# Kernel optimization log

Hardware: AMD Instinct MI355X
Metric: run time of the kernel (lower is better)

The kernel has to match this reference:

```python
import jax, jax.numpy as jnp
import numpy as np

B, C, H, V = 16384, 5, 256, 512
NUM_ITER = 2


def setup_inputs() -> dict:
    key = jax.random.key(0)
    k1, k2, k3, k4 = jax.random.split(key, 4)
    # v0: one-hot categorical visible units, shape [B, C, V, 1]
    idx = jax.random.randint(k1, (B, V), 0, C)
    v0 = jax.nn.one_hot(idx, C, axis=1, dtype=jnp.float32)[..., None]
    W = 0.01 * jax.random.normal(k2, (C, H, V), dtype=jnp.float32)
    b = 0.01 * jax.random.normal(k3, (C, V, 1), dtype=jnp.float32)
    c = 0.01 * jax.random.normal(k4, (H, 1), dtype=jnp.float32)
    return {"v0": v0, "W": W, "b": b, "c": c, "num_sampling_iter": NUM_ITER}


def reference(v0, W, b, c, num_sampling_iter):
    key = jax.random.key(42)
    b2 = b[..., 0]   # [C, V]
    c1 = c[:, 0]     # [H]
    v = v0[..., 0]   # [B, C, V]

    def sample_h(k, v):
        # p(h=1|v) = sigmoid(sum_c W[c] @ v[:,c] + c)
        p = jax.nn.sigmoid(jnp.einsum('chv,bcv->bh', W, v) + c1)  # [B, H]
        return jax.random.bernoulli(k, p).astype(v.dtype)

    def sample_v(k, h):
        # logits over categories per visible unit: W[c].T @ h + b[c]
        logits = jnp.einsum('chv,bh->bcv', W, h) + b2  # [B, C, V]
        idx = jax.random.categorical(k, logits, axis=1)  # [B, V]
        return jax.nn.one_hot(idx, C, axis=1, dtype=h.dtype)  # [B, C, V]

    keys = jax.random.split(key, 2 * num_sampling_iter + 1)
    h = sample_h(keys[0], v)
    h_given_v0 = h
    for i in range(num_sampling_iter):  # small fixed iteration count
        v = sample_v(keys[2 * i + 1], h)
        h = sample_h(keys[2 * i + 2], v)
    return (v[..., None], h[..., None], h_given_v0[..., None])
```

## Files before the change

kernel.cpp:

```cpp
#include <hip/hip_runtime.h>
#include <cstdint>
#include <cstddef>


#define B_DIM 16384
#define C_DIM 5
#define H_DIM 256
#define V_DIM 512
#define KC    320

struct TFOut { uint32_t a, b; };

typedef float f32x2 __attribute__((ext_vector_type(2)));

#if __has_builtin(__builtin_elementwise_fma)
#define PKFMA(A, B, C) __builtin_elementwise_fma((A), (B), (C))
#else
static __device__ inline f32x2 pkfma_(f32x2 a, f32x2 b, f32x2 c) {
  f32x2 r; r.x = fmaf(a.x, b.x, c.x); r.y = fmaf(a.y, b.y, c.y); return r;
}
#define PKFMA(A, B, C) pkfma_((A), (B), (C))
#endif

__host__ __device__ static inline TFOut tf2x32(uint32_t k0, uint32_t k1,
                                               uint32_t c0, uint32_t c1) {
  uint32_t ks2 = k0 ^ k1 ^ 0x1BD11BDAu;
  uint32_t x0 = c0 + k0, x1 = c1 + k1;
#define TF_R(r) { x0 += x1; x1 = (x1 << r) | (x1 >> (32 - r)); x1 ^= x0; }
  TF_R(13) TF_R(15) TF_R(26) TF_R(6)
  x0 += k1;  x1 += ks2 + 1u;
  TF_R(17) TF_R(29) TF_R(16) TF_R(24)
  x0 += ks2; x1 += k0 + 2u;
  TF_R(13) TF_R(15) TF_R(26) TF_R(6)
  x0 += k0;  x1 += k1 + 3u;
  TF_R(17) TF_R(29) TF_R(16) TF_R(24)
  x0 += k1;  x1 += ks2 + 4u;
  TF_R(13) TF_R(15) TF_R(26) TF_R(6)
  x0 += ks2; x1 += k0 + 5u;
#undef TF_R
  TFOut o; o.a = x0; o.b = x1; return o;
}

__device__ static inline uint32_t rng_bits(uint32_t k0, uint32_t k1, uint32_t i) {
  TFOut r = tf2x32(k0, k1, 0u, i);
  return r.a ^ r.b;
}

__device__ static inline float bits_to_unit_float(uint32_t bits) {
  return __uint_as_float((bits >> 9) | 0x3F800000u) - 1.0f;
}

__device__ static float xla_exp(float x_in) {
#pragma clang fp contract(off)
  float x = fminf(x_in, 88.3762626647950f);
  x = fmaxf(x, -88.3762626647949f);
  float fx = floorf(x * 1.44269504088896341f + 0.5f);
  float tmp = fx * 0.693359375f;
  float z = fx * -2.12194440e-4f;
  x = x - tmp;
  x = x - z;
  z = x * x;
  float y = 1.9875691500e-4f;
  y = y * x + 1.3981999507e-3f;
  y = y * x + 8.3334519073e-3f;
  y = y * x + 4.1665795894e-2f;
  y = y * x + 1.6666665459e-1f;
  y = y * x + 5.0000001201e-1f;
  y = y * z + x;
  y = y + 1.0f;
  int n = (int)fx;
  y = y * __uint_as_float((uint32_t)(n + 127) << 23);
  return y;
}

__device__ static float xla_log(float x_in) {
#pragma clang fp contract(off)
  float xv = fmaxf(x_in, 1.17549435e-38f);
  uint32_t bits = __float_as_uint(xv);
  float e = (float)((int)(bits >> 23) - 126);
  float x = __uint_as_float((bits & 0x007FFFFFu) | 0x3F000000u);
  bool m = (x < 0.707106781186547524f);
  float tmp = m ? x : 0.0f;
  x = x - 1.0f;
  e = e - (m ? 1.0f : 0.0f);
  x = x + tmp;
  float z = x * x;
  float y = 7.0376836292e-2f;
  y = y * x + -1.1514610310e-1f;
  y = y * x + 1.1676998740e-1f;
  y = y * x + -1.2420140846e-1f;
  y = y * x + 1.4249322787e-1f;
  y = y * x + -1.6668057665e-1f;
  y = y * x + 2.0000714765e-1f;
  y = y * x + -2.4999993993e-1f;
  y = y * x + 3.3333331174e-1f;
  y = y * x;
  y = y * z;
  float t1 = e * -2.12194440e-4f;
  y = y + t1;
  float t2 = z * 0.5f;
  y = y - t2;
  x = x + y;
  float t3 = e * 0.693359375f;
  x = x + t3;
  return x;
}


__global__ void k_sentinel(float* out, float d) {
  out[0] = d;
}

__global__ __launch_bounds__(256) void k_idx(const float* __restrict__ v0,
                                             uint8_t* __restrict__ idx) {
  int t = blockIdx.x * 256 + threadIdx.x;
  int b = t >> 9, v = t & 511;
  const float* p = v0 + (size_t)b * (C_DIM * V_DIM) + v;
  int cf = 0;
#pragma unroll
  for (int c = 0; c < C_DIM; ++c)
    if (p[c * V_DIM] > 0.5f) cf = c;
  idx[t] = (uint8_t)cf;
}

__global__ __launch_bounds__(256) void k_wt(const float* __restrict__ W,
                                            float* __restrict__ Wt) {
  int t = blockIdx.x * 256 + threadIdx.x;
  int h = t & 255; int rest = t >> 8; int v = rest & 511; int c = rest >> 9;
  Wt[t] = W[((size_t)c * H_DIM + h) * V_DIM + v];
}

__global__ __launch_bounds__(256) void k_sample_h(
    const float* __restrict__ Wt, const float* __restrict__ c1,
    const uint8_t* __restrict__ idx,
    float* __restrict__ out_h, uint32_t* __restrict__ out_mask,
    uint32_t key0, uint32_t key1) {
  __shared__ uint8_t  sidx[V_DIM];
  __shared__ uint32_t soff[V_DIM];
  __shared__ uint16_t cnt[8][5];
  __shared__ uint16_t base[8][5];
  __shared__ uint16_t jb[10];
  int b = blockIdx.x;
  int t = threadIdx.x;
  if (t < 128)
    ((uint32_t*)sidx)[t] = ((const uint32_t*)(idx + (size_t)b * V_DIM))[t];
  __syncthreads();

  int lane = t & 63, wv = t >> 6;
  int v0 = t,       c0 = sidx[v0];
  int v1 = t + 256, c1i = sidx[v1];
  int rank0, rank1;
  {
    unsigned long long bal[5];
#pragma unroll
    for (int cc = 0; cc < 5; ++cc) bal[cc] = __ballot(c0 == cc);
    if (lane == 0) {
#pragma unroll
      for (int cc = 0; cc < 5; ++cc) cnt[wv][cc] = (uint16_t)__popcll(bal[cc]);
    }
    rank0 = (int)__popcll(bal[c0] & ((1ull << lane) - 1ull));
  }
  {
    unsigned long long bal[5];
#pragma unroll
    for (int cc = 0; cc < 5; ++cc) bal[cc] = __ballot(c1i == cc);
    if (lane == 0) {
#pragma unroll
      for (int cc = 0; cc < 5; ++cc) cnt[4 + wv][cc] = (uint16_t)__popcll(bal[cc]);
    }
    rank1 = (int)__popcll(bal[c1i] & ((1ull << lane) - 1ull));
  }
  __syncthreads();
  if (t == 0) {
    int pos = 0;
    for (int cc = 0; cc < 5; ++cc)
      for (int g = 0; g < 8; ++g) { base[g][cc] = (uint16_t)pos; pos += cnt[g][cc]; }
  }
  __syncthreads();
  soff[base[wv][c0] + rank0]       = (uint32_t)(c0 * V_DIM + v0) << 10;
  soff[base[4 + wv][c1i] + rank1]  = (uint32_t)(c1i * V_DIM + v1) << 10;
  __syncthreads();
  if (t < 10) {
    uint32_t target = (uint32_t)(t * KC) << 10;
    int lo = 0, hi = V_DIM;
    while (lo < hi) { int mid = (lo + hi) >> 1;
      if (soff[mid] < target) lo = mid + 1; else hi = mid; }
    jb[t] = (uint16_t)lo;
  }
  __syncthreads();

  const char* Wh = (const char*)Wt + (size_t)t * 4;
  float total = 0.0f;
  for (int s = 0; s < 9; ++s) {
    int j = jb[s], jend = jb[s + 1];
    float psum = 0.0f;
    for (; j + 4 <= jend; j += 4) {
      float w0 = *(const float*)(Wh + soff[j]);
      float w1 = *(const float*)(Wh + soff[j + 1]);
      float w2 = *(const float*)(Wh + soff[j + 2]);
      float w3 = *(const float*)(Wh + soff[j + 3]);
      psum += w0; psum += w1; psum += w2; psum += w3;
    }
    for (; j < jend; ++j) psum += *(const float*)(Wh + soff[j]);
    total += psum;
  }

  float tt = total + c1[t];
  float p = 1.0f / (1.0f + xla_exp(-tt));

  uint32_t i = (uint32_t)(b * H_DIM + t);
  float u = bits_to_unit_float(rng_bits(key0, key1, i));
  bool hb = (u < p);
  if (out_h) out_h[(size_t)b * H_DIM + t] = hb ? 1.0f : 0.0f;

  unsigned long long m = __ballot(hb);
  if ((t & 63) == 0) {
    out_mask[(size_t)b * 8 + wv * 2 + 0] = (uint32_t)(m & 0xFFFFFFFFull);
    out_mask[(size_t)b * 8 + wv * 2 + 1] = (uint32_t)(m >> 32);
  }
}

#define ACC_H(BITS, W4)                                              \
  {                                                                  \
    f32x2 w01 = {(W4).x, (W4).y}, w23 = {(W4).z, (W4).w};            \
    uint32_t bits_ = (BITS) >> (bgrp * 8);                           \
    _Pragma("unroll")                                                \
    for (int i = 0; i < 8; ++i) {                                    \
      float f = (float)((bits_ >> i) & 1u);                          \
      f32x2 ff = {f, f};                                             \
      a01[i] = PKFMA(w01, ff, a01[i]);                               \
      a23[i] = PKFMA(w23, ff, a23[i]);                               \
    }                                                                \
  }

__global__ __launch_bounds__(256, 4) void k_sample_v(
    const float* __restrict__ W, const float* __restrict__ b2,
    const uint32_t* __restrict__ mask, uint8_t* __restrict__ idx_out,
    uint32_t key0, uint32_t key1) {
  __shared__ uint32_t smask[16][8];
  __shared__ __align__(16) uint32_t tb[H_DIM];
  int tid = threadIdx.x;
  int b0 = blockIdx.x * 16;

  if (tid < 128) smask[tid >> 3][tid & 7] = mask[(size_t)b0 * 8 + tid];
  __syncthreads();
  {
    int h = tid;
    uint32_t w = (uint32_t)(h >> 5), s = (uint32_t)(h & 31), x = 0;
#pragma unroll
    for (int j = 0; j < 16; ++j)
      x |= ((smask[j][w] >> s) & 1u) << j;
    tb[h] = x;
  }
  __syncthreads();

  int wv = tid >> 6, lane = tid & 63;
  int bgrp = wv & 1, vhalf = wv >> 1;
  int b_base = b0 + bgrp * 8;
  int v0 = vhalf * 256 + lane * 4;

  float best[8][4];
  uint32_t bc[8];
#pragma unroll
  for (int i = 0; i < 8; ++i) bc[i] = 0u;

  const uint4* tbv = (const uint4*)tb;

  for (int c = 0; c < C_DIM; ++c) {
    f32x2 a01[8], a23[8];
#pragma unroll
    for (int i = 0; i < 8; ++i) {
      a01[i] = (f32x2){0.0f, 0.0f};
      a23[i] = (f32x2){0.0f, 0.0f};
    }
    const float* wp = W + (size_t)c * (H_DIM * V_DIM) + v0;
    uint4 qn = tbv[0];
    for (int h4 = 0; h4 < 64; ++h4) {
      uint4 qq = qn;
      if (h4 < 63) qn = tbv[h4 + 1];
      float4 w0 = *(const float4*)(wp);
      float4 w1 = *(const float4*)(wp + V_DIM);
      float4 w2 = *(const float4*)(wp + 2 * V_DIM);
      float4 w3 = *(const float4*)(wp + 3 * V_DIM);
      wp += 4 * V_DIM;
      ACC_H(qq.x, w0)
      ACC_H(qq.y, w1)
      ACC_H(qq.z, w2)
      ACC_H(qq.w, w3)
    }

    float4 bv = *(const float4*)(b2 + c * V_DIM + v0);
    float bb0 = bv.x, bb1 = bv.y, bb2 = bv.z, bb3 = bv.w;
#pragma unroll
    for (int i = 0; i < 8; ++i) {
      uint32_t ib = ((uint32_t)(b_base + i) * C_DIM + (uint32_t)c) * V_DIM
                    + (uint32_t)v0;
      float av[4] = {a01[i].x, a01[i].y, a23[i].x, a23[i].y};
      float bbq[4] = {bb0, bb1, bb2, bb3};
#pragma unroll
      for (int q = 0; q < 4; ++q) {
        float uf = bits_to_unit_float(rng_bits(key0, key1, ib + (uint32_t)q));
        if (uf == 0.0f) uf = 1.17549435e-38f;
        float g = -xla_log(-xla_log(uf));
        float z = g + (av[q] + bbq[q]);
        if (c == 0 || z > best[i][q]) {
          best[i][q] = z;
          bc[i] = (bc[i] & ~(0xFFu << (8 * q))) | ((uint32_t)c << (8 * q));
        }
      }
    }
  }

#pragma unroll
  for (int i = 0; i < 8; ++i)
    *(uint32_t*)(idx_out + (size_t)(b_base + i) * V_DIM + v0) = bc[i];
}

__global__ __launch_bounds__(256) void k_onehot(const uint8_t* __restrict__ idx,
                                                float* __restrict__ out) {
  int t = blockIdx.x * 256 + threadIdx.x;
  int v = t & 511; int rest = t >> 9; int c = rest % C_DIM; int b = rest / C_DIM;
  out[t] = (idx[(size_t)b * V_DIM + v] == c) ? 1.0f : 0.0f;
}


extern "C" void kernel_launch(void* const* d_in, const int* in_sizes, int n_in,
                              void* d_out, int out_size, void* d_ws, size_t ws_size,
                              hipStream_t stream) {
  float* out = (float*)d_out;

  const size_t WS_NEED = 2621440ull
                       + 2621440ull
                       + 8388608ull
                       + 524288ull;
  float D = 0.0f;
  if (n_in < 4)                       D = 910.0f + (float)n_in;
  else if (in_sizes[0] != 41943040)   D = 920.0f;
  else if (in_sizes[1] != 655360)     D = 921.0f;
  else if (in_sizes[2] != 2560)       D = 922.0f;
  else if (in_sizes[3] != 256)        D = 923.0f;
  else if (out_size != 50331648)      D = 930.0f + (float)out_size * 1e-6f;
  else if (ws_size < WS_NEED)         D = 100.0f + (float)(ws_size >> 20);
  if (D != 0.0f) {
    hipLaunchKernelGGL(k_sentinel, dim3(1), dim3(1), 0, stream, out, D);
    return;
  }

  const float* v0 = (const float*)d_in[0];
  const float* W  = (const float*)d_in[1];
  const float* b2 = (const float*)d_in[2];
  const float* c1 = (const float*)d_in[3];

  float* out_v  = out;
  float* out_h  = out + (size_t)B_DIM * C_DIM * V_DIM;
  float* out_h0 = out_h + (size_t)B_DIM * H_DIM;

  char* ws = (char*)d_ws;
  float*    Wt   = (float*)(ws);
  uint8_t*  idx  = (uint8_t*)(ws + 5242880);
  uint32_t* mask = (uint32_t*)(ws + 13631488);

  uint32_t keys[5][2];
  for (int i = 0; i < 5; ++i) {
    TFOut r = tf2x32(0u, 42u, 0u, (uint32_t)i);
    keys[i][0] = r.a; keys[i][1] = r.b;
  }

  hipLaunchKernelGGL(k_wt,  dim3(2560),  dim3(256), 0, stream, W, Wt);
  hipLaunchKernelGGL(k_idx, dim3(32768), dim3(256), 0, stream, v0, idx);

  hipLaunchKernelGGL(k_sample_h, dim3(B_DIM), dim3(256), 0, stream,
                     Wt, c1, idx, out_h0, mask, keys[0][0], keys[0][1]);
  hipLaunchKernelGGL(k_sample_v, dim3(B_DIM / 16), dim3(256), 0, stream,
                     W, b2, mask, idx, keys[1][0], keys[1][1]);
  hipLaunchKernelGGL(k_sample_h, dim3(B_DIM), dim3(256), 0, stream,
                     Wt, c1, idx, (float*)nullptr, mask, keys[2][0], keys[2][1]);
  hipLaunchKernelGGL(k_sample_v, dim3(B_DIM / 16), dim3(256), 0, stream,
                     W, b2, mask, idx, keys[3][0], keys[3][1]);
  hipLaunchKernelGGL(k_sample_h, dim3(B_DIM), dim3(256), 0, stream,
                     Wt, c1, idx, out_h, mask, keys[4][0], keys[4][1]);
  hipLaunchKernelGGL(k_onehot, dim3(163840), dim3(256), 0, stream, idx, out_v);
}
```

Before: 2.223 ms.

## Tile sample_h over 16-row batches with shared W slabs; split sample_v into GEMM and Gumbel

k_sample_h now handles 16 batch rows and half of H per block. It streams Wt through double-buffered shared-memory slabs so each weight chunk is reused across 16 rows instead of gathered per row from global memory. sample_v is split into a plain GEMM kernel that writes the logits into the output buffer, followed by a separate elementwise Gumbel-argmax kernel. This trades the fused compute for extra global traffic on an intermediate of about 168 MB. The new h kernel's per-row while loops over shared memory and its many syncs may introduce divergence and barrier overhead.

```diff
diff --git a/kernel.cpp b/kernel.cpp
--- a/kernel.cpp
+++ b/kernel.cpp
@@ -7,20 +7,8 @@
 #define C_DIM 5
 #define H_DIM 256
 #define V_DIM 512
-#define KC    320
 
 struct TFOut { uint32_t a, b; };
-
-typedef float f32x2 __attribute__((ext_vector_type(2)));
-
-#if __has_builtin(__builtin_elementwise_fma)
-#define PKFMA(A, B, C) __builtin_elementwise_fma((A), (B), (C))
-#else
-static __device__ inline f32x2 pkfma_(f32x2 a, f32x2 b, f32x2 c) {
-  f32x2 r; r.x = fmaf(a.x, b.x, c.x); r.y = fmaf(a.y, b.y, c.y); return r;
-}
-#define PKFMA(A, B, C) pkfma_((A), (B), (C))
-#endif
 
 __host__ __device__ static inline TFOut tf2x32(uint32_t k0, uint32_t k1,
                                                uint32_t c0, uint32_t c1) {
@@ -130,190 +118,238 @@
   Wt[t] = W[((size_t)c * H_DIM + h) * V_DIM + v];
 }
 
-__global__ __launch_bounds__(256) void k_sample_h(
-    const float* __restrict__ Wt, const float* __restrict__ c1,
+__global__ __launch_bounds__(256, 4) void k_sample_h(
+    const float* __restrict__ Wt, const float* __restrict__ c1g,
     const uint8_t* __restrict__ idx,
     float* __restrict__ out_h, uint32_t* __restrict__ out_mask,
     uint32_t key0, uint32_t key1) {
   __shared__ uint8_t  sidx[V_DIM];
-  __shared__ uint32_t soff[V_DIM];
+  __shared__ uint16_t soff[16][V_DIM];
+  __shared__ __align__(16) float slab[2][16 * 128];
   __shared__ uint16_t cnt[8][5];
   __shared__ uint16_t base[8][5];
-  __shared__ uint16_t jb[10];
-  int b = blockIdx.x;
+  __shared__ uint32_t hb32[16][4];
+
   int t = threadIdx.x;
-  if (t < 128)
-    ((uint32_t*)sidx)[t] = ((const uint32_t*)(idx + (size_t)b * V_DIM))[t];
+  int bb = blockIdx.x >> 1, hh = blockIdx.x & 1;
+  int b0 = bb * 16, h0 = hh * 128;
+  int wv = t >> 6, lane = t & 63;
+
+  for (int bi = 0; bi < 16; ++bi) {
+    if (t < 128)
+      ((uint32_t*)sidx)[t] =
+          ((const uint32_t*)(idx + (size_t)(b0 + bi) * V_DIM))[t];
+    __syncthreads();
+    int v0 = t, c0 = sidx[v0];
+    int v1 = t + 256, c1i = sidx[v1];
+    int rank0, rank1;
+    {
+      unsigned long long bal[5];
+#pragma unroll
+      for (int cc = 0; cc < 5; ++cc) bal[cc] = __ballot(c0 == cc);
+      if (lane == 0) {
+#pragma unroll
+        for (int cc = 0; cc < 5; ++cc) cnt[wv][cc] = (uint16_t)__popcll(bal[cc]);
+      }
+      rank0 = (int)__popcll(bal[c0] & ((1ull << lane) - 1ull));
+    }
+    {
+      unsigned long long bal[5];
+#pragma unroll
+      for (int cc = 0; cc < 5; ++cc) bal[cc] = __ballot(c1i == cc);
+      if (lane == 0) {
+#pragma unroll
+        for (int cc = 0; cc < 5; ++cc) cnt[4 + wv][cc] = (uint16_t)__popcll(bal[cc]);
+      }
+      rank1 = (int)__popcll(bal[c1i] & ((1ull << lane) - 1ull));
+    }
+    __syncthreads();
+    if (t == 0) {
+      int pos = 0;
+      for (int cc = 0; cc < 5; ++cc)
+        for (int gg = 0; gg < 8; ++gg) { base[gg][cc] = (uint16_t)pos; pos += cnt[gg][cc]; }
+    }
+    __syncthreads();
+    soff[bi][base[wv][c0] + rank0]      = (uint16_t)(c0 * V_DIM + v0);
+    soff[bi][base[4 + wv][c1i] + rank1] = (uint16_t)(c1i * V_DIM + v1);
+    __syncthreads();
+  }
+
+  float ps0[4], ps1[4], tt0[4], tt1[4];
+  int jp[4];
+#pragma unroll
+  for (int i = 0; i < 4; ++i) {
+    ps0[i] = 0.f; ps1[i] = 0.f; tt0[i] = 0.f; tt1[i] = 0.f; jp[i] = 0;
+  }
+
+  {
+    int p = t * 4;
+    int row = p >> 7, off = p & 127;
+    const float* s = Wt + (size_t)row * H_DIM + h0 + off;
+    float4 r0 = *(const float4*)s;
+    float4 r1 = *(const float4*)(s + 8 * H_DIM);
+    *(float4*)&slab[0][row * 128 + off] = r0;
+    *(float4*)&slab[0][(row + 8) * 128 + off] = r1;
+  }
   __syncthreads();
 
-  int lane = t & 63, wv = t >> 6;
-  int v0 = t,       c0 = sidx[v0];
-  int v1 = t + 256, c1i = sidx[v1];
-  int rank0, rank1;
-  {
-    unsigned long long bal[5];
-#pragma unroll
-    for (int cc = 0; cc < 5; ++cc) bal[cc] = __ballot(c0 == cc);
-    if (lane == 0) {
-#pragma unroll
-      for (int cc = 0; cc < 5; ++cc) cnt[wv][cc] = (uint16_t)__popcll(bal[cc]);
-    }
-    rank0 = (int)__popcll(bal[c0] & ((1ull << lane) - 1ull));
-  }
-  {
-    unsigned long long bal[5];
-#pragma unroll
-    for (int cc = 0; cc < 5; ++cc) bal[cc] = __ballot(c1i == cc);
-    if (lane == 0) {
-#pragma unroll
-      for (int cc = 0; cc < 5; ++cc) cnt[4 + wv][cc] = (uint16_t)__popcll(bal[cc]);
-    }
-    rank1 = (int)__popcll(bal[c1i] & ((1ull << lane) - 1ull));
-  }
+  for (int ch = 0; ch < 160; ++ch) {
+    int buf = ch & 1;
+    float4 r0, r1; int row = 0, off = 0;
+    bool pre = (ch + 1 < 160);
+    if (pre) {
+      int p = t * 4;
+      row = p >> 7; off = p & 127;
+      const float* s = Wt + ((size_t)(ch + 1) * 16 + row) * H_DIM + h0 + off;
+      r0 = *(const float4*)s;
+      r1 = *(const float4*)(s + 8 * H_DIM);
+    }
+    if ((ch % 20) == 0) {
+#pragma unroll
+      for (int i = 0; i < 4; ++i) {
+        tt0[i] = tt0[i] + ps0[i]; ps0[i] = 0.f;
+        tt1[i] = tt1[i] + ps1[i]; ps1[i] = 0.f;
+      }
+    }
+    int kend = ch * 16 + 16;
+#pragma unroll
+    for (int i = 0; i < 4; ++i) {
+      int bi = wv * 4 + i;
+      int j = jp[i];
+      float p0 = ps0[i], p1 = ps1[i];
+      while (j < 512) {
+        int k = soff[bi][j];
+        if (k >= kend) break;
+        const float* wp = &slab[buf][(k & 15) * 128 + (lane << 1)];
+        float2 w2 = *(const float2*)wp;
+        p0 += w2.x;
+        p1 += w2.y;
+        ++j;
+      }
+      ps0[i] = p0; ps1[i] = p1; jp[i] = j;
+    }
+    __syncthreads();
+    if (pre) {
+      *(float4*)&slab[buf ^ 1][row * 128 + off] = r0;
+      *(float4*)&slab[buf ^ 1][(row + 8) * 128 + off] = r1;
+    }
+    __syncthreads();
+  }
+#pragma unroll
+  for (int i = 0; i < 4; ++i) {
+    tt0[i] = tt0[i] + ps0[i];
+    tt1[i] = tt1[i] + ps1[i];
+  }
+
+  if (t < 64) ((uint32_t*)hb32)[t] = 0u;
   __syncthreads();
-  if (t == 0) {
-    int pos = 0;
-    for (int cc = 0; cc < 5; ++cc)
-      for (int g = 0; g < 8; ++g) { base[g][cc] = (uint16_t)pos; pos += cnt[g][cc]; }
+  float2 c1v = *(const float2*)&c1g[h0 + (lane << 1)];
+  int h = h0 + (lane << 1);
+#pragma unroll
+  for (int i = 0; i < 4; ++i) {
+    int b = b0 + wv * 4 + i;
+    float ta = tt0[i] + c1v.x;
+    float tb = tt1[i] + c1v.y;
+    float pa = 1.0f / (1.0f + xla_exp(-ta));
+    float pb = 1.0f / (1.0f + xla_exp(-tb));
+    float ua = bits_to_unit_float(rng_bits(key0, key1, (uint32_t)(b * H_DIM + h)));
+    float ub = bits_to_unit_float(rng_bits(key0, key1, (uint32_t)(b * H_DIM + h + 1)));
+    bool ha = ua < pa, hb = ub < pb;
+    if (out_h) {
+      float2 o; o.x = ha ? 1.0f : 0.0f; o.y = hb ? 1.0f : 0.0f;
+      *(float2*)&out_h[(size_t)b * H_DIM + h] = o;
+    }
+    uint32_t bitpos = (uint32_t)((lane << 1) & 31);
+    uint32_t val = ((ha ? 1u : 0u) << bitpos) | ((hb ? 1u : 0u) << (bitpos + 1));
+    atomicOr(&hb32[wv * 4 + i][lane >> 4], val);
   }
   __syncthreads();
-  soff[base[wv][c0] + rank0]       = (uint32_t)(c0 * V_DIM + v0) << 10;
-  soff[base[4 + wv][c1i] + rank1]  = (uint32_t)(c1i * V_DIM + v1) << 10;
-  __syncthreads();
-  if (t < 10) {
-    uint32_t target = (uint32_t)(t * KC) << 10;
-    int lo = 0, hi = V_DIM;
-    while (lo < hi) { int mid = (lo + hi) >> 1;
-      if (soff[mid] < target) lo = mid + 1; else hi = mid; }
-    jb[t] = (uint16_t)lo;
-  }
-  __syncthreads();
-
-  const char* Wh = (const char*)Wt + (size_t)t * 4;
-  float total = 0.0f;
-  for (int s = 0; s < 9; ++s) {
-    int j = jb[s], jend = jb[s + 1];
-    float psum = 0.0f;
-    for (; j + 4 <= jend; j += 4) {
-      float w0 = *(const float*)(Wh + soff[j]);
-      float w1 = *(const float*)(Wh + soff[j + 1]);
-      float w2 = *(const float*)(Wh + soff[j + 2]);
-      float w3 = *(const float*)(Wh + soff[j + 3]);
-      psum += w0; psum += w1; psum += w2; psum += w3;
-    }
-    for (; j < jend; ++j) psum += *(const float*)(Wh + soff[j]);
-    total += psum;
-  }
-
-  float tt = total + c1[t];
-  float p = 1.0f / (1.0f + xla_exp(-tt));
-
-  uint32_t i = (uint32_t)(b * H_DIM + t);
-  float u = bits_to_unit_float(rng_bits(key0, key1, i));
-  bool hb = (u < p);
-  if (out_h) out_h[(size_t)b * H_DIM + t] = hb ? 1.0f : 0.0f;
-
-  unsigned long long m = __ballot(hb);
-  if ((t & 63) == 0) {
-    out_mask[(size_t)b * 8 + wv * 2 + 0] = (uint32_t)(m & 0xFFFFFFFFull);
-    out_mask[(size_t)b * 8 + wv * 2 + 1] = (uint32_t)(m >> 32);
-  }
-}
-
-#define ACC_H(BITS, W4)                                              \
-  {                                                                  \
-    f32x2 w01 = {(W4).x, (W4).y}, w23 = {(W4).z, (W4).w};            \
-    uint32_t bits_ = (BITS) >> (bgrp * 8);                           \
-    _Pragma("unroll")                                                \
-    for (int i = 0; i < 8; ++i) {                                    \
-      float f = (float)((bits_ >> i) & 1u);                          \
-      f32x2 ff = {f, f};                                             \
-      a01[i] = PKFMA(w01, ff, a01[i]);                               \
-      a23[i] = PKFMA(w23, ff, a23[i]);                               \
-    }                                                                \
-  }
-
-__global__ __launch_bounds__(256, 4) void k_sample_v(
-    const float* __restrict__ W, const float* __restrict__ b2,
-    const uint32_t* __restrict__ mask, uint8_t* __restrict__ idx_out,
-    uint32_t key0, uint32_t key1) {
+  if (t < 64) {
+    int bl = t >> 2, wl = t & 3;
+    out_mask[(size_t)(b0 + bl) * 8 + hh * 4 + wl] = hb32[bl][wl];
+  }
+}
+
+#define GEMM_PAIR(i, F)                      \
+  a0[i] = fmaf(w2.x, F, a0[i]);              \
+  a1[i] = fmaf(w2.y, F, a1[i]);
+
+__global__ __launch_bounds__(256, 4) void k_gemm_v(
+    const float* __restrict__ W, const uint32_t* __restrict__ mask,
+    float* __restrict__ sums) {
   __shared__ uint32_t smask[16][8];
-  __shared__ __align__(16) uint32_t tb[H_DIM];
-  int tid = threadIdx.x;
+  __shared__ __align__(16) float tbf[H_DIM][16];
+  int t = threadIdx.x;
   int b0 = blockIdx.x * 16;
-
-  if (tid < 128) smask[tid >> 3][tid & 7] = mask[(size_t)b0 * 8 + tid];
+  if (t < 128) smask[t >> 3][t & 7] = mask[(size_t)b0 * 8 + t];
   __syncthreads();
   {
-    int h = tid;
+    int h = t;
     uint32_t w = (uint32_t)(h >> 5), s = (uint32_t)(h & 31), x = 0;
 #pragma unroll
     for (int j = 0; j < 16; ++j)
       x |= ((smask[j][w] >> s) & 1u) << j;
-    tb[h] = x;
+#pragma unroll
+    for (int i = 0; i < 16; ++i)
+      tbf[h][i] = (float)((x >> i) & 1u);
   }
   __syncthreads();
 
-  int wv = tid >> 6, lane = tid & 63;
-  int bgrp = wv & 1, vhalf = wv >> 1;
-  int b_base = b0 + bgrp * 8;
-  int v0 = vhalf * 256 + lane * 4;
-
-  float best[8][4];
-  uint32_t bc[8];
-#pragma unroll
-  for (int i = 0; i < 8; ++i) bc[i] = 0u;
-
-  const uint4* tbv = (const uint4*)tb;
+  int wv = t >> 6, lane = t & 63;
+  int v0 = wv * 128 + (lane << 1);
 
   for (int c = 0; c < C_DIM; ++c) {
-    f32x2 a01[8], a23[8];
-#pragma unroll
-    for (int i = 0; i < 8; ++i) {
-      a01[i] = (f32x2){0.0f, 0.0f};
-      a23[i] = (f32x2){0.0f, 0.0f};
-    }
+    float a0[16], a1[16];
+#pragma unroll
+    for (int i = 0; i < 16; ++i) { a0[i] = 0.f; a1[i] = 0.f; }
     const float* wp = W + (size_t)c * (H_DIM * V_DIM) + v0;
-    uint4 qn = tbv[0];
-    for (int h4 = 0; h4 < 64; ++h4) {
-      uint4 qq = qn;
-      if (h4 < 63) qn = tbv[h4 + 1];
-      float4 w0 = *(const float4*)(wp);
-      float4 w1 = *(const float4*)(wp + V_DIM);
-      float4 w2 = *(const float4*)(wp + 2 * V_DIM);
-      float4 w3 = *(const float4*)(wp + 3 * V_DIM);
-      wp += 4 * V_DIM;
-      ACC_H(qq.x, w0)
-      ACC_H(qq.y, w1)
-      ACC_H(qq.z, w2)
-      ACC_H(qq.w, w3)
-    }
-
-    float4 bv = *(const float4*)(b2 + c * V_DIM + v0);
-    float bb0 = bv.x, bb1 = bv.y, bb2 = bv.z, bb3 = bv.w;
-#pragma unroll
-    for (int i = 0; i < 8; ++i) {
-      uint32_t ib = ((uint32_t)(b_base + i) * C_DIM + (uint32_t)c) * V_DIM
-                    + (uint32_t)v0;
-      float av[4] = {a01[i].x, a01[i].y, a23[i].x, a23[i].y};
-      float bbq[4] = {bb0, bb1, bb2, bb3};
-#pragma unroll
-      for (int q = 0; q < 4; ++q) {
-        float uf = bits_to_unit_float(rng_bits(key0, key1, ib + (uint32_t)q));
-        if (uf == 0.0f) uf = 1.17549435e-38f;
-        float g = -xla_log(-xla_log(uf));
-        float z = g + (av[q] + bbq[q]);
-        if (c == 0 || z > best[i][q]) {
-          best[i][q] = z;
-          bc[i] = (bc[i] & ~(0xFFu << (8 * q))) | ((uint32_t)c << (8 * q));
-        }
+#pragma unroll 2
+    for (int h = 0; h < H_DIM; ++h) {
+      float2 w2 = *(const float2*)wp;
+      wp += V_DIM;
+      const float4* fp = (const float4*)&tbf[h][0];
+      float4 fA = fp[0], fB = fp[1], fC = fp[2], fD = fp[3];
+      GEMM_PAIR(0,  fA.x) GEMM_PAIR(1,  fA.y) GEMM_PAIR(2,  fA.z) GEMM_PAIR(3,  fA.w)
+      GEMM_PAIR(4,  fB.x) GEMM_PAIR(5,  fB.y) GEMM_PAIR(6,  fB.z) GEMM_PAIR(7,  fB.w)
+      GEMM_PAIR(8,  fC.x) GEMM_PAIR(9,  fC.y) GEMM_PAIR(10, fC.z) GEMM_PAIR(11, fC.w)
+      GEMM_PAIR(12, fD.x) GEMM_PAIR(13, fD.y) GEMM_PAIR(14, fD.z) GEMM_PAIR(15, fD.w)
+    }
+#pragma unroll
+    for (int i = 0; i < 16; ++i) {
+      float2 o; o.x = a0[i]; o.y = a1[i];
+      *(float2*)&sums[((size_t)c * B_DIM + b0 + i) * V_DIM + v0] = o;
+    }
+  }
+}
+
+__global__ __launch_bounds__(256, 4) void k_gumbel_v(
+    const float* __restrict__ sums, const float* __restrict__ b2,
+    uint8_t* __restrict__ idx_out, uint32_t key0, uint32_t key1) {
+  int gidx = blockIdx.x * 256 + threadIdx.x;
+  int b = gidx >> 7;
+  int v0 = (gidx & 127) << 2;
+  float best[4];
+  uint32_t bc = 0;
+#pragma unroll
+  for (int c = 0; c < C_DIM; ++c) {
+    float4 av = *(const float4*)&sums[((size_t)c * B_DIM + b) * V_DIM + v0];
+    float4 bv = *(const float4*)&b2[c * V_DIM + v0];
+    uint32_t ib = ((uint32_t)b * C_DIM + (uint32_t)c) * V_DIM + (uint32_t)v0;
+    float avq[4] = {av.x, av.y, av.z, av.w};
+    float bvq[4] = {bv.x, bv.y, bv.z, bv.w};
+#pragma unroll
+    for (int q = 0; q < 4; ++q) {
+      float uf = bits_to_unit_float(rng_bits(key0, key1, ib + (uint32_t)q));
+      if (uf == 0.0f) uf = 1.17549435e-38f;
+      float gz = -xla_log(-xla_log(uf));
+      float z = gz + (avq[q] + bvq[q]);
+      if (c == 0 || z > best[q]) {
+        best[q] = z;
+        bc = (bc & ~(0xFFu << (8 * q))) | ((uint32_t)c << (8 * q));
       }
     }
   }
-
-#pragma unroll
-  for (int i = 0; i < 8; ++i)
-    *(uint32_t*)(idx_out + (size_t)(b_base + i) * V_DIM + v0) = bc[i];
+  *(uint32_t*)(idx_out + (size_t)b * V_DIM + v0) = bc;
 }
 
 __global__ __launch_bounds__(256) void k_onehot(const uint8_t* __restrict__ idx,
@@ -360,6 +396,8 @@
   uint8_t*  idx  = (uint8_t*)(ws + 5242880);
   uint32_t* mask = (uint32_t*)(ws + 13631488);
 
+  float* sums = out_v;
+
   uint32_t keys[5][2];
   for (int i = 0; i < 5; ++i) {
     TFOut r = tf2x32(0u, 42u, 0u, (uint32_t)i);
@@ -369,15 +407,19 @@
   hipLaunchKernelGGL(k_wt,  dim3(2560),  dim3(256), 0, stream, W, Wt);
   hipLaunchKernelGGL(k_idx, dim3(32768), dim3(256), 0, stream, v0, idx);
 
-  hipLaunchKernelGGL(k_sample_h, dim3(B_DIM), dim3(256), 0, stream,
+  hipLaunchKernelGGL(k_sample_h, dim3(B_DIM / 16 * 2), dim3(256), 0, stream,
                      Wt, c1, idx, out_h0, mask, keys[0][0], keys[0][1]);
-  hipLaunchKernelGGL(k_sample_v, dim3(B_DIM / 16), dim3(256), 0, stream,
-                     W, b2, mask, idx, keys[1][0], keys[1][1]);
-  hipLaunchKernelGGL(k_sample_h, dim3(B_DIM), dim3(256), 0, stream,
+  hipLaunchKernelGGL(k_gemm_v, dim3(B_DIM / 16), dim3(256), 0, stream,
+                     W, mask, sums);
+  hipLaunchKernelGGL(k_gumbel_v, dim3(B_DIM * 128 / 256), dim3(256), 0, stream,
+                     sums, b2, idx, keys[1][0], keys[1][1]);
+  hipLaunchKernelGGL(k_sample_h, dim3(B_DIM / 16 * 2), dim3(256), 0, stream,
                      Wt, c1, idx, (float*)nullptr, mask, keys[2][0], keys[2][1]);
-  hipLaunchKernelGGL(k_sample_v, dim3(B_DIM / 16), dim3(256), 0, stream,
-                     W, b2, mask, idx, keys[3][0], keys[3][1]);
-  hipLaunchKernelGGL(k_sample_h, dim3(B_DIM), dim3(256), 0, stream,
+  hipLaunchKernelGGL(k_gemm_v, dim3(B_DIM / 16), dim3(256), 0, stream,
+                     W, mask, sums);
+  hipLaunchKernelGGL(k_gumbel_v, dim3(B_DIM * 128 / 256), dim3(256), 0, stream,
+                     sums, b2, idx, keys[3][0], keys[3][1]);
+  hipLaunchKernelGGL(k_sample_h, dim3(B_DIM / 16 * 2), dim3(256), 0, stream,
                      Wt, c1, idx, out_h, mask, keys[4][0], keys[4][1]);
   hipLaunchKernelGGL(k_onehot, dim3(163840), dim3(256), 0, stream, idx, out_v);
 }
```

New measurement: 4.401 ms. +98.0%, slower.

## Split visible-unit sampling into separate GEMM and Gumbel-argmax kernels

Applied to the files above, without the earlier changes.

The fused sample_v kernel is split in two. A GEMM kernel expands the hidden bit masks into float tiles in shared memory and accumulates W^T h with packed FMAs, 2 v-columns by 16 batches per thread, then writes the logits to a scratch buffer that reuses the output region. A second elementwise kernel adds the bias, generates Gumbel noise and takes the argmax. This separates the RNG and transcendental work from the FMA loop to reduce register pressure and improve the GEMM's throughput. The cost is writing and rereading a 160 MB logits buffer per iteration, plus shared-memory float loads in place of bit extraction.

```diff
diff --git a/kernel.cpp b/kernel.cpp
--- a/kernel.cpp
+++ b/kernel.cpp
@@ -12,15 +12,19 @@
 struct TFOut { uint32_t a, b; };
 
 typedef float f32x2 __attribute__((ext_vector_type(2)));
-
+typedef float f32x4 __attribute__((ext_vector_type(4)));
+
+static __device__ inline f32x2 mk2(float x, float y) {
+  f32x2 r; r.x = x; r.y = y; return r;
+}
+
+static __device__ inline f32x2 pkfma(f32x2 a, f32x2 b, f32x2 c) {
 #if __has_builtin(__builtin_elementwise_fma)
-#define PKFMA(A, B, C) __builtin_elementwise_fma((A), (B), (C))
+  return __builtin_elementwise_fma(a, b, c);
 #else
-static __device__ inline f32x2 pkfma_(f32x2 a, f32x2 b, f32x2 c) {
   f32x2 r; r.x = fmaf(a.x, b.x, c.x); r.y = fmaf(a.y, b.y, c.y); return r;
-}
-#define PKFMA(A, B, C) pkfma_((A), (B), (C))
 #endif
+}
 
 __host__ __device__ static inline TFOut tf2x32(uint32_t k0, uint32_t k1,
                                                uint32_t c0, uint32_t c1) {
@@ -220,100 +224,109 @@
   }
 }
 
-#define ACC_H(BITS, W4)                                              \
-  {                                                                  \
-    f32x2 w01 = {(W4).x, (W4).y}, w23 = {(W4).z, (W4).w};            \
-    uint32_t bits_ = (BITS) >> (bgrp * 8);                           \
-    _Pragma("unroll")                                                \
-    for (int i = 0; i < 8; ++i) {                                    \
-      float f = (float)((bits_ >> i) & 1u);                          \
-      f32x2 ff = {f, f};                                             \
-      a01[i] = PKFMA(w01, ff, a01[i]);                               \
-      a23[i] = PKFMA(w23, ff, a23[i]);                               \
-    }                                                                \
-  }
-
-__global__ __launch_bounds__(256, 4) void k_sample_v(
-    const float* __restrict__ W, const float* __restrict__ b2,
-    const uint32_t* __restrict__ mask, uint8_t* __restrict__ idx_out,
-    uint32_t key0, uint32_t key1) {
+static __device__ inline void gv_h(float2 w2, const float* tbf_row,
+                                   f32x2* av0, f32x2* av1) {
+  f32x2 ww0 = mk2(w2.x, w2.x);
+  f32x2 ww1 = mk2(w2.y, w2.y);
+  const f32x4* fp = (const f32x4*)tbf_row;
+  f32x4 qA = fp[0], qB = fp[1], qC = fp[2], qD = fp[3];
+  f32x2 f0 = __builtin_shufflevector(qA, qA, 0, 1);
+  f32x2 f1 = __builtin_shufflevector(qA, qA, 2, 3);
+  f32x2 f2 = __builtin_shufflevector(qB, qB, 0, 1);
+  f32x2 f3 = __builtin_shufflevector(qB, qB, 2, 3);
+  f32x2 f4 = __builtin_shufflevector(qC, qC, 0, 1);
+  f32x2 f5 = __builtin_shufflevector(qC, qC, 2, 3);
+  f32x2 f6 = __builtin_shufflevector(qD, qD, 0, 1);
+  f32x2 f7 = __builtin_shufflevector(qD, qD, 2, 3);
+  av0[0] = pkfma(ww0, f0, av0[0]); av1[0] = pkfma(ww1, f0, av1[0]);
+  av0[1] = pkfma(ww0, f1, av0[1]); av1[1] = pkfma(ww1, f1, av1[1]);
+  av0[2] = pkfma(ww0, f2, av0[2]); av1[2] = pkfma(ww1, f2, av1[2]);
+  av0[3] = pkfma(ww0, f3, av0[3]); av1[3] = pkfma(ww1, f3, av1[3]);
+  av0[4] = pkfma(ww0, f4, av0[4]); av1[4] = pkfma(ww1, f4, av1[4]);
+  av0[5] = pkfma(ww0, f5, av0[5]); av1[5] = pkfma(ww1, f5, av1[5]);
+  av0[6] = pkfma(ww0, f6, av0[6]); av1[6] = pkfma(ww1, f6, av1[6]);
+  av0[7] = pkfma(ww0, f7, av0[7]); av1[7] = pkfma(ww1, f7, av1[7]);
+}
+
+__global__ __launch_bounds__(256, 4) void k_gemm_v(
+    const float* __restrict__ W, const uint32_t* __restrict__ mask,
+    float* __restrict__ sums) {
   __shared__ uint32_t smask[16][8];
-  __shared__ __align__(16) uint32_t tb[H_DIM];
-  int tid = threadIdx.x;
+  __shared__ __align__(16) float tbf[H_DIM][16];
+  int t = threadIdx.x;
   int b0 = blockIdx.x * 16;
-
-  if (tid < 128) smask[tid >> 3][tid & 7] = mask[(size_t)b0 * 8 + tid];
+  if (t < 128) smask[t >> 3][t & 7] = mask[(size_t)b0 * 8 + t];
   __syncthreads();
   {
-    int h = tid;
+    int h = t;
     uint32_t w = (uint32_t)(h >> 5), s = (uint32_t)(h & 31), x = 0;
 #pragma unroll
     for (int j = 0; j < 16; ++j)
       x |= ((smask[j][w] >> s) & 1u) << j;
-    tb[h] = x;
-  }
-  __syncthreads();
-
-  int wv = tid >> 6, lane = tid & 63;
-  int bgrp = wv & 1, vhalf = wv >> 1;
-  int b_base = b0 + bgrp * 8;
-  int v0 = vhalf * 256 + lane * 4;
-
-  float best[8][4];
-  uint32_t bc[8];
-#pragma unroll
-  for (int i = 0; i < 8; ++i) bc[i] = 0u;
-
-  const uint4* tbv = (const uint4*)tb;
+#pragma unroll
+    for (int i = 0; i < 16; ++i)
+      tbf[h][i] = (float)((x >> i) & 1u);
+  }
+  __syncthreads();
+
+  int wv = t >> 6, lane = t & 63;
+  int v0 = wv * 128 + (lane << 1);
 
   for (int c = 0; c < C_DIM; ++c) {
-    f32x2 a01[8], a23[8];
-#pragma unroll
-    for (int i = 0; i < 8; ++i) {
-      a01[i] = (f32x2){0.0f, 0.0f};
-      a23[i] = (f32x2){0.0f, 0.0f};
+    f32x2 av0[8], av1[8];
+#pragma unroll
+    for (int j = 0; j < 8; ++j) {
+      av0[j] = mk2(0.f, 0.f);
+      av1[j] = mk2(0.f, 0.f);
     }
     const float* wp = W + (size_t)c * (H_DIM * V_DIM) + v0;
-    uint4 qn = tbv[0];
-    for (int h4 = 0; h4 < 64; ++h4) {
-      uint4 qq = qn;
-      if (h4 < 63) qn = tbv[h4 + 1];
-      float4 w0 = *(const float4*)(wp);
-      float4 w1 = *(const float4*)(wp + V_DIM);
-      float4 w2 = *(const float4*)(wp + 2 * V_DIM);
-      float4 w3 = *(const float4*)(wp + 3 * V_DIM);
-      wp += 4 * V_DIM;
-      ACC_H(qq.x, w0)
-      ACC_H(qq.y, w1)
-      ACC_H(qq.z, w2)
-      ACC_H(qq.w, w3)
-    }
-
-    float4 bv = *(const float4*)(b2 + c * V_DIM + v0);
-    float bb0 = bv.x, bb1 = bv.y, bb2 = bv.z, bb3 = bv.w;
-#pragma unroll
-    for (int i = 0; i < 8; ++i) {
-      uint32_t ib = ((uint32_t)(b_base + i) * C_DIM + (uint32_t)c) * V_DIM
-                    + (uint32_t)v0;
-      float av[4] = {a01[i].x, a01[i].y, a23[i].x, a23[i].y};
-      float bbq[4] = {bb0, bb1, bb2, bb3};
-#pragma unroll
-      for (int q = 0; q < 4; ++q) {
-        float uf = bits_to_unit_float(rng_bits(key0, key1, ib + (uint32_t)q));
-        if (uf == 0.0f) uf = 1.17549435e-38f;
-        float g = -xla_log(-xla_log(uf));
-        float z = g + (av[q] + bbq[q]);
-        if (c == 0 || z > best[i][q]) {
-          best[i][q] = z;
-          bc[i] = (bc[i] & ~(0xFFu << (8 * q))) | ((uint32_t)c << (8 * q));
-        }
+    for (int hh = 0; hh < H_DIM; hh += 8) {
+      float2 w8[8];
+#pragma unroll
+      for (int u = 0; u < 8; ++u)
+        w8[u] = *(const float2*)(wp + (size_t)(hh + u) * V_DIM);
+#pragma unroll
+      for (int u = 0; u < 8; ++u)
+        gv_h(w8[u], &tbf[hh + u][0], av0, av1);
+    }
+#pragma unroll
+    for (int j = 0; j < 8; ++j) {
+      float2 oA; oA.x = av0[j].x; oA.y = av1[j].x;
+      *(float2*)&sums[((size_t)c * B_DIM + b0 + 2 * j) * V_DIM + v0] = oA;
+      float2 oB; oB.x = av0[j].y; oB.y = av1[j].y;
+      *(float2*)&sums[((size_t)c * B_DIM + b0 + 2 * j + 1) * V_DIM + v0] = oB;
+    }
+  }
+}
+
+__global__ __launch_bounds__(256, 4) void k_gumbel_v(
+    const float* __restrict__ sums, const float* __restrict__ b2,
+    uint8_t* __restrict__ idx_out, uint32_t key0, uint32_t key1) {
+  int gidx = blockIdx.x * 256 + threadIdx.x;
+  int b = gidx >> 7;
+  int v0 = (gidx & 127) << 2;
+  float best[4];
+  uint32_t bc = 0;
+#pragma unroll
+  for (int c = 0; c < C_DIM; ++c) {
+    float4 av = *(const float4*)&sums[((size_t)c * B_DIM + b) * V_DIM + v0];
+    float4 bv = *(const float4*)&b2[c * V_DIM + v0];
+    uint32_t ib = ((uint32_t)b * C_DIM + (uint32_t)c) * V_DIM + (uint32_t)v0;
+    float avq[4] = {av.x, av.y, av.z, av.w};
+    float bvq[4] = {bv.x, bv.y, bv.z, bv.w};
+#pragma unroll
+    for (int q = 0; q < 4; ++q) {
+      float uf = bits_to_unit_float(rng_bits(key0, key1, ib + (uint32_t)q));
+      if (uf == 0.0f) uf = 1.17549435e-38f;
+      float gz = -xla_log(-xla_log(uf));
+      float z = gz + (avq[q] + bvq[q]);
+      if (c == 0 || z > best[q]) {
+        best[q] = z;
+        bc = (bc & ~(0xFFu << (8 * q))) | ((uint32_t)c << (8 * q));
       }
     }
   }
-
-#pragma unroll
-  for (int i = 0; i < 8; ++i)
-    *(uint32_t*)(idx_out + (size_t)(b_base + i) * V_DIM + v0) = bc[i];
+  *(uint32_t*)(idx_out + (size_t)b * V_DIM + v0) = bc;
 }
 
 __global__ __launch_bounds__(256) void k_onehot(const uint8_t* __restrict__ idx,
@@ -360,6 +373,8 @@
   uint8_t*  idx  = (uint8_t*)(ws + 5242880);
   uint32_t* mask = (uint32_t*)(ws + 13631488);
 
+  float* sums = out_v;
+
   uint32_t keys[5][2];
   for (int i = 0; i < 5; ++i) {
     TFOut r = tf2x32(0u, 42u, 0u, (uint32_t)i);
@@ -371,12 +386,16 @@
 
   hipLaunchKernelGGL(k_sample_h, dim3(B_DIM), dim3(256), 0, stream,
                      Wt, c1, idx, out_h0, mask, keys[0][0], keys[0][1]);
-  hipLaunchKernelGGL(k_sample_v, dim3(B_DIM / 16), dim3(256), 0, stream,
-                     W, b2, mask, idx, keys[1][0], keys[1][1]);
+  hipLaunchKernelGGL(k_gemm_v, dim3(B_DIM / 16), dim3(256), 0, stream,
+                     W, mask, sums);
+  hipLaunchKernelGGL(k_gumbel_v, dim3(B_DIM * 128 / 256), dim3(256), 0, stream,
+                     sums, b2, idx, keys[1][0], keys[1][1]);
   hipLaunchKernelGGL(k_sample_h, dim3(B_DIM), dim3(256), 0, stream,
                      Wt, c1, idx, (float*)nullptr, mask, keys[2][0], keys[2][1]);
-  hipLaunchKernelGGL(k_sample_v, dim3(B_DIM / 16), dim3(256), 0, stream,
-                     W, b2, mask, idx, keys[3][0], keys[3][1]);
+  hipLaunchKernelGGL(k_gemm_v, dim3(B_DIM / 16), dim3(256), 0, stream,
+                     W, mask, sums);
+  hipLaunchKernelGGL(k_gumbel_v, dim3(B_DIM * 128 / 256), dim3(256), 0, stream,
+                     sums, b2, idx, keys[3][0], keys[3][1]);
   hipLaunchKernelGGL(k_sample_h, dim3(B_DIM), dim3(256), 0, stream,
                      Wt, c1, idx, out_h, mask, keys[4][0], keys[4][1]);
   hipLaunchKernelGGL(k_onehot, dim3(163840), dim3(256), 0, stream, idx, out_v);
```

Measured after the change: 2.033 ms. -8.6%, faster.
